# Kernel tuning notes

Hardware: AMD Instinct MI355X
Metric: run time of the kernel (lower is better)

Reference implementation:

```python
import jax, jax.numpy as jnp
import numpy as np

H = 16  # num_attention_heads


def setup_inputs() -> dict:
    key = jax.random.key(0)
    k1, k2, k3 = jax.random.split(key, 3)
    B, S, E = 2, 2048, 1024
    return {
        "hidden_states": jax.random.normal(k1, (B, S, E), dtype=jnp.float32),
        "W_attn": jax.random.normal(k2, (E, 3 * E), dtype=jnp.float32) * 0.02,
        "b_attn": jnp.zeros((3 * E,), dtype=jnp.float32),
        "W_proj": jax.random.normal(k3, (E, E), dtype=jnp.float32) * 0.02,
        "b_proj": jnp.zeros((E,), dtype=jnp.float32),
    }


def reference(hidden_states, W_attn, b_attn, W_proj, b_proj):
    B, S, E = hidden_states.shape
    hd = E // H
    # Conv1D: x @ W + b -> [B, S, 3E]
    qkv = hidden_states @ W_attn + b_attn
    # Faithful to module: _split_heads with 3*head_dim FIRST, then split q/k/v.
    # i.e. per-head slice of size 3*hd is [q_h | k_h | v_h] (interleaved layout).
    qkv = qkv.reshape(B, S, H, 3 * hd).transpose(0, 2, 1, 3)  # [B, H, S, 3*hd]
    q, k, v = jnp.split(qkv, 3, axis=-1)                      # each [B, H, S, hd]
    # scores, scaled by sqrt(head_dim) (value.size(-1) ** 0.5)
    scores = jnp.einsum("bhqd,bhkd->bhqk", q, k) / jnp.asarray(hd, q.dtype) ** 0.5
    # causal mask via where with masked_bias = -10000.0 (not -inf), as in module
    causal = jnp.tril(jnp.ones((S, S), dtype=bool))
    scores = jnp.where(causal, scores, jnp.asarray(-10000.0, scores.dtype))
    attn_weights = jax.nn.softmax(scores, axis=-1)  # dropout p=0 -> identity
    attn_out = jnp.einsum("bhqk,bhkd->bhqd", attn_weights, v)
    attn_out = attn_out.transpose(0, 2, 1, 3).reshape(B, S, E)  # merge heads
    return attn_out @ W_proj + b_proj
```

## Files before the change

### kernel.cpp

```cpp
#include <hip/hip_runtime.h>
#include <hip/hip_bf16.h>


typedef __attribute__((ext_vector_type(4))) float f32x4;
typedef __attribute__((ext_vector_type(8))) short short8;
typedef __attribute__((ext_vector_type(2))) unsigned int uint2v;

#define AS1 __attribute__((address_space(1)))
#define AS3 __attribute__((address_space(3)))

__device__ __forceinline__ void load_lds16(const void* g, void* l) {
    __builtin_amdgcn_global_load_lds((const AS1 void*)g, (AS3 void*)l, 16, 0, 0);
}

__device__ __forceinline__ unsigned short f2bf(float f) {
    union { float f; unsigned int u; } v; v.f = f;
    unsigned int r = v.u + 0x7FFFu + ((v.u >> 16) & 1u);
    return (unsigned short)(r >> 16);
}

__device__ __forceinline__ int cvt_pk_bf16(float lo, float hi) {
    int r;
    asm("v_cvt_pk_bf16_f32 %0, %1, %2" : "=v"(r) : "v"(lo), "v"(hi));
    return r;
}

__device__ __forceinline__ void transpose_tile(
    const float* __restrict__ W, unsigned short* __restrict__ Wt,
    int K, int N, int bx, int by, int t) {
    __shared__ float tile[32][33];
    int k0 = by * 32, n0 = bx * 32;
    int r = t >> 3, c = (t & 7) * 4;
    float4 v = *(const float4*)&W[(size_t)(k0 + r) * N + n0 + c];
    tile[r][c] = v.x; tile[r][c + 1] = v.y; tile[r][c + 2] = v.z; tile[r][c + 3] = v.w;
    __syncthreads();
    int n = t >> 3; int kk = (t & 7) * 4;
    ushort4 o;
    o.x = f2bf(tile[kk + 0][n]);
    o.y = f2bf(tile[kk + 1][n]);
    o.z = f2bf(tile[kk + 2][n]);
    o.w = f2bf(tile[kk + 3][n]);
    *(ushort4*)&Wt[(size_t)(n0 + n) * K + k0 + kk] = o;
}

__global__ __launch_bounds__(256) void prep(
    const float* __restrict__ hs, unsigned short* __restrict__ Xb,
    const float* __restrict__ W_attn, unsigned short* __restrict__ WaT,
    const float* __restrict__ W_proj, unsigned short* __restrict__ WpT) {
    int bid = blockIdx.x, t = threadIdx.x;
    if (bid < 4096) {
        int i = (bid * 256 + t) * 4;
        float4 v = *(const float4*)(hs + i);
        ushort4 o;
        o.x = f2bf(v.x); o.y = f2bf(v.y); o.z = f2bf(v.z); o.w = f2bf(v.w);
        *(ushort4*)(Xb + i) = o;
    } else if (bid < 7168) {
        int r = bid - 4096;
        transpose_tile(W_attn, WaT, 1024, 3072, r % 96, r / 96, t);
    } else {
        int r = bid - 7168;
        transpose_tile(W_proj, WpT, 1024, 1024, r % 32, r / 32, t);
    }
}

__global__ __launch_bounds__(256) void gemm_qkv(
    const unsigned short* __restrict__ A,
    const unsigned short* __restrict__ Bt,
    const float* __restrict__ bias,
    unsigned short* __restrict__ qk, unsigned short* __restrict__ Vt,
    int M, int N, int K) {
    __shared__ unsigned short Sh[8704];
    unsigned short* As = Sh;
    unsigned short* Bs = Sh + 4096;
    unsigned short* Tb = Sh;
    const int t = threadIdx.x, wave = t >> 6, lane = t & 63;
    const int l15 = lane & 15, quad = lane >> 4;
    const int m0 = blockIdx.y * 128, n0 = blockIdx.x * 128;
    const int srow = wave * 32 + (lane >> 2);
    const int sch = (lane & 3) * 8;
    const unsigned short* Ag = A + (size_t)(m0 + srow) * K + sch;
    const unsigned short* Bg = Bt + (size_t)(n0 + srow) * K + sch;
    unsigned short* AsW = &As[wave * 32 * 32];
    unsigned short* BsW = &Bs[wave * 32 * 32];
    const int wm = (wave >> 1) * 64, wn = (wave & 1) * 64;
    f32x4 acc[4][4] = {};
    for (int k0 = 0; k0 < K; k0 += 32) {
        load_lds16(Ag + k0, AsW);
        load_lds16(Ag + k0 + (size_t)16 * K, AsW + 16 * 32);
        load_lds16(Bg + k0, BsW);
        load_lds16(Bg + k0 + (size_t)16 * K, BsW + 16 * 32);
        __syncthreads();
        short8 af[4], bf[4];
#pragma unroll
        for (int i = 0; i < 4; ++i) {
            af[i] = *(const short8*)&As[(wm + i * 16 + l15) * 32 + quad * 8];
            bf[i] = *(const short8*)&Bs[(wn + i * 16 + l15) * 32 + quad * 8];
        }
#pragma unroll
        for (int mt = 0; mt < 4; ++mt)
#pragma unroll
            for (int nt = 0; nt < 4; ++nt)
                acc[mt][nt] = __builtin_amdgcn_mfma_f32_16x16x32_bf16(af[mt], bf[nt], acc[mt][nt], 0, 0, 0);
        __syncthreads();
    }
    const int rem = n0 % 192;
#pragma unroll
    for (int mt = 0; mt < 4; ++mt) {
        int mrow = m0 + wm + mt * 16 + quad * 4;
#pragma unroll
        for (int nt = 0; nt < 4; ++nt) {
            int col = n0 + wn + nt * 16 + l15;
            float bv = bias[col];
            int h = col / 192;
            int j = col - h * 192;
            if (j < 128) {
                float sc = (j < 64) ? 0.125f : 1.0f;
#pragma unroll
                for (int r = 0; r < 4; ++r)
                    qk[(size_t)(mrow + r) * 2048 + h * 128 + j] = f2bf((acc[mt][nt][r] + bv) * sc);
            } else {
                int d = j - 128;
                int s_local = wm + mt * 16 + quad * 4;
                ushort4 pk;
                pk.x = f2bf(acc[mt][nt][0] + bv);
                pk.y = f2bf(acc[mt][nt][1] + bv);
                pk.z = f2bf(acc[mt][nt][2] + bv);
                pk.w = f2bf(acc[mt][nt][3] + bv);
                *(ushort4*)&Tb[d * 136 + s_local] = pk;
            }
        }
    }
    if (rem != 0) {
        __syncthreads();
        int vhalf = (rem == 64) ? 1 : 0;
        int h = (n0 + vhalf * 64) / 192;
        int b = m0 >> 11;
        unsigned short* vbase = Vt + ((size_t)(b * 16 + h) * 64) * 2048 + (m0 & 2047);
        int drow = t >> 4, ch = (t & 15) * 8;
#pragma unroll
        for (int rr = 0; rr < 4; ++rr) {
            int d = rr * 16 + drow;
            *(uint4*)(vbase + (size_t)d * 2048 + ch) = *(const uint4*)&Tb[d * 136 + ch];
        }
    }
}

__global__ __launch_bounds__(256) void gemm_proj(
    const unsigned short* __restrict__ A,
    const unsigned short* __restrict__ Bt,
    const float* __restrict__ bias,
    float* __restrict__ C, int M, int N, int K) {
    __shared__ unsigned short As[128 * 32];
    __shared__ unsigned short Bs[64 * 32];
    const int t = threadIdx.x, wave = t >> 6, lane = t & 63;
    const int l15 = lane & 15, quad = lane >> 4;
    const int m0 = blockIdx.y * 128, n0 = blockIdx.x * 64;
    const int srowA = wave * 32 + (lane >> 2);
    const int sch = (lane & 3) * 8;
    const unsigned short* Ag = A + (size_t)(m0 + srowA) * K + sch;
    const unsigned short* Bg = Bt + (size_t)(n0 + wave * 16 + (lane >> 2)) * K + sch;
    unsigned short* AsW = &As[wave * 32 * 32];
    unsigned short* BsW = &Bs[wave * 16 * 32];
    const int wm = (wave >> 1) * 64, wn = (wave & 1) * 32;
    f32x4 acc[4][2] = {};
    for (int k0 = 0; k0 < K; k0 += 32) {
        load_lds16(Ag + k0, AsW);
        load_lds16(Ag + k0 + (size_t)16 * K, AsW + 16 * 32);
        load_lds16(Bg + k0, BsW);
        __syncthreads();
        short8 af[4], bf[2];
#pragma unroll
        for (int i = 0; i < 4; ++i)
            af[i] = *(const short8*)&As[(wm + i * 16 + l15) * 32 + quad * 8];
#pragma unroll
        for (int i = 0; i < 2; ++i)
            bf[i] = *(const short8*)&Bs[(wn + i * 16 + l15) * 32 + quad * 8];
#pragma unroll
        for (int mt = 0; mt < 4; ++mt)
#pragma unroll
            for (int nt = 0; nt < 2; ++nt)
                acc[mt][nt] = __builtin_amdgcn_mfma_f32_16x16x32_bf16(af[mt], bf[nt], acc[mt][nt], 0, 0, 0);
        __syncthreads();
    }
#pragma unroll
    for (int mt = 0; mt < 4; ++mt) {
        int mrow = m0 + wm + mt * 16 + quad * 4;
#pragma unroll
        for (int nt = 0; nt < 2; ++nt) {
            int col = n0 + wn + nt * 16 + l15;
            float bv = bias[col];
#pragma unroll
            for (int r = 0; r < 4; ++r)
                C[(size_t)(mrow + r) * N + col] = acc[mt][nt][r] + bv;
        }
    }
}

__device__ __forceinline__ void build_af(const int (&pk)[4][2], int qpar, short8 (&af)[2]) {
#pragma unroll
    for (int km = 0; km < 2; ++km) {
        uint2v r0 = __builtin_amdgcn_permlane32_swap(
            (unsigned)pk[2 * km][0], (unsigned)pk[2 * km + 1][0], false, false);
        uint2v r1 = __builtin_amdgcn_permlane32_swap(
            (unsigned)pk[2 * km][1], (unsigned)pk[2 * km + 1][1], false, false);
        int Ap0 = (int)r0[0], Bp0 = (int)r0[1];
        int Ap1 = (int)r1[0], Bp1 = (int)r1[1];
        int z0 = qpar ? Ap0 : Bp0;
        int z1 = qpar ? Ap1 : Bp1;
        int w0 = __builtin_amdgcn_ds_swizzle(z0, 0x401F);
        int w1 = __builtin_amdgcn_ds_swizzle(z1, 0x401F);
        int f0 = qpar ? w0 : Ap0, f1 = qpar ? w1 : Ap1;
        int g0 = qpar ? Bp0 : w0, g1 = qpar ? Bp1 : w1;
        int4 v = {f0, f1, g0, g1};
        af[km] = __builtin_bit_cast(short8, v);
    }
}

__global__ __launch_bounds__(512, 4) void attn3(
    const unsigned short* __restrict__ qk,
    const unsigned short* __restrict__ Vt,
    unsigned short* __restrict__ out) {
    const int S = 2048;
    __shared__ unsigned short Ks[2][64][72];
    __shared__ unsigned short Vts[2][64][72];
    const int t = threadIdx.x, wave = t >> 6, lane = t & 63;
    const int l15 = lane & 15, quad = lane >> 4, qpar = quad & 1;
    const int bid = blockIdx.x;
    const int qt = (bid < 256) ? (15 - (bid >> 5)) : ((bid - 256) >> 5);
    const int bh = bid & 31;
    const int b = bh >> 4, h = bh & 15;
    const unsigned short* qkb = qk + (size_t)b * S * 2048 + h * 128;
    const unsigned short* vtb = Vt + (size_t)bh * 64 * 2048;

    const int q0 = qt * 128 + wave * 16;
    short8 qf[2];
#pragma unroll
    for (int km = 0; km < 2; ++km)
        qf[km] = *(const short8*)(qkb + (size_t)(q0 + l15) * 2048 + km * 32 + quad * 8);
    f32x4 o[4] = {};
    float lrun = 0.f;

    const int srow8 = t >> 3, chunk8 = (t & 7) * 8;
    const int KT = qt * 2 + 2;

    uint4 kreg = *(const uint4*)(qkb + (size_t)srow8 * 2048 + 64 + chunk8);
    uint4 vreg = *(const uint4*)(vtb + (size_t)srow8 * 2048 + chunk8);

    const int qg = q0 + l15;
    const int qmax = q0 + 15;

    for (int kt = 0; kt < KT; ++kt) {
        const int cur = kt & 1;
        *(uint4*)&Ks[cur][srow8][chunk8] = kreg;
        *(uint4*)&Vts[cur][srow8][chunk8] = vreg;
        __syncthreads();
        if (kt + 1 < KT) {
            int kn = (kt + 1) * 64;
            kreg = *(const uint4*)(qkb + (size_t)(kn + srow8) * 2048 + 64 + chunk8);
            vreg = *(const uint4*)(vtb + (size_t)srow8 * 2048 + kn + chunk8);
        }
        const int kb = kt * 64;
        if (kb > qmax) continue;

        f32x4 s[4] = {};
        __builtin_amdgcn_s_setprio(1);
#pragma unroll
        for (int km = 0; km < 2; ++km)
#pragma unroll
            for (int nt = 0; nt < 4; ++nt) {
                short8 kf = *(const short8*)&Ks[cur][nt * 16 + l15][km * 32 + quad * 8];
                s[nt] = __builtin_amdgcn_mfma_f32_16x16x32_bf16(kf, qf[km], s[nt], 0, 0, 0);
            }
        __builtin_amdgcn_s_setprio(0);

        if (kb + 63 > q0) {
            const int ka = kb + quad * 4;
#pragma unroll
            for (int nt = 0; nt < 4; ++nt)
#pragma unroll
                for (int r = 0; r < 4; ++r)
                    if (ka + nt * 16 + r > qg) s[nt][r] = -1e30f;
        }

        int pk[4][2];
        float a0 = 0.f;
#pragma unroll
        for (int nt = 0; nt < 4; ++nt) {
            float pa[4];
#pragma unroll
            for (int r = 0; r < 4; ++r) {
                pa[r] = __expf(s[nt][r]);
                a0 += pa[r];
            }
            pk[nt][0] = cvt_pk_bf16(pa[0], pa[1]);
            pk[nt][1] = cvt_pk_bf16(pa[2], pa[3]);
        }
        lrun += a0;

        short8 af[2];
        build_af(pk, qpar, af);

        __builtin_amdgcn_s_setprio(1);
#pragma unroll
        for (int km = 0; km < 2; ++km)
#pragma unroll
            for (int nt = 0; nt < 4; ++nt) {
                short8 vf = *(const short8*)&Vts[cur][nt * 16 + l15][km * 32 + quad * 8];
                o[nt] = __builtin_amdgcn_mfma_f32_16x16x32_bf16(af[km], vf, o[nt], 0, 0, 0);
            }
        __builtin_amdgcn_s_setprio(0);
    }

    float t0 = lrun + __shfl_xor(lrun, 16);
    t0 += __shfl_xor(t0, 32);
    unsigned short* ob = out + (size_t)b * S * 1024 + h * 64;
#pragma unroll
    for (int r = 0; r < 4; ++r) {
        float i0 = 1.0f / __shfl(t0, quad * 4 + r);
        size_t r0 = (size_t)(q0 + quad * 4 + r) * 1024;
#pragma unroll
        for (int nt = 0; nt < 4; ++nt)
            ob[r0 + nt * 16 + l15] = f2bf(o[nt][r] * i0);
    }
}

extern "C" void kernel_launch(void* const* d_in, const int* in_sizes, int n_in,
                              void* d_out, int out_size, void* d_ws, size_t ws_size,
                              hipStream_t stream) {
    const float* hs     = (const float*)d_in[0];
    const float* W_attn = (const float*)d_in[1];
    const float* b_attn = (const float*)d_in[2];
    const float* W_proj = (const float*)d_in[3];
    const float* b_proj = (const float*)d_in[4];
    float* out = (float*)d_out;

    const int B = 2, S = 2048, E = 1024;
    const int M = B * S;
    const int N3 = 3 * E;

    unsigned short* Xb  = (unsigned short*)d_ws;
    unsigned short* WaT = Xb + (size_t)M * E;
    unsigned short* WpT = WaT + (size_t)N3 * E;
    unsigned short* qkb = WpT + (size_t)E * E;
    unsigned short* Vt  = qkb + (size_t)M * 2048;
    unsigned short* ao  = Vt + (size_t)M * E;

    prep<<<dim3(8192), 256, 0, stream>>>(hs, Xb, W_attn, WaT, W_proj, WpT);

    gemm_qkv<<<dim3(N3 / 128, M / 128), 256, 0, stream>>>(Xb, WaT, b_attn, qkb, Vt, M, N3, E);

    attn3<<<dim3(512), 512, 0, stream>>>(qkb, Vt, ao);

    gemm_proj<<<dim3(E / 64, M / 128), 256, 0, stream>>>(ao, WpT, b_proj, out, M, E, E);
}
```

Before: 184.0 us.

## Double-buffer LDS tiles in QKV and projection GEMMs with MFMA priority boost

Both GEMM kernels now keep two LDS buffers. The next K-slice is fetched with async global-to-LDS loads while MFMAs run on the current slice, so each K step needs one barrier instead of two. The MFMA block is wrapped in s_setprio to favour matrix issue over other waves. The cost is roughly twice the LDS per block, which can lower occupancy. An extra barrier after the QKV loop protects reuse of the LDS transpose buffer.

```diff
diff --git a/kernel.cpp b/kernel.cpp
--- a/kernel.cpp
+++ b/kernel.cpp
@@ -69,10 +69,8 @@
     const float* __restrict__ bias,
     unsigned short* __restrict__ qk, unsigned short* __restrict__ Vt,
     int M, int N, int K) {
-    __shared__ unsigned short Sh[8704];
-    unsigned short* As = Sh;
-    unsigned short* Bs = Sh + 4096;
-    unsigned short* Tb = Sh;
+    __shared__ unsigned short Sh[2][8192];
+    unsigned short* Tb = &Sh[0][0];
     const int t = threadIdx.x, wave = t >> 6, lane = t & 63;
     const int l15 = lane & 15, quad = lane >> 4;
     const int m0 = blockIdx.y * 128, n0 = blockIdx.x * 128;
@@ -80,29 +78,43 @@
     const int sch = (lane & 3) * 8;
     const unsigned short* Ag = A + (size_t)(m0 + srow) * K + sch;
     const unsigned short* Bg = Bt + (size_t)(n0 + srow) * K + sch;
-    unsigned short* AsW = &As[wave * 32 * 32];
-    unsigned short* BsW = &Bs[wave * 32 * 32];
+    const int wOff = wave * 1024;
     const int wm = (wave >> 1) * 64, wn = (wave & 1) * 64;
     f32x4 acc[4][4] = {};
-    for (int k0 = 0; k0 < K; k0 += 32) {
-        load_lds16(Ag + k0, AsW);
-        load_lds16(Ag + k0 + (size_t)16 * K, AsW + 16 * 32);
-        load_lds16(Bg + k0, BsW);
-        load_lds16(Bg + k0 + (size_t)16 * K, BsW + 16 * 32);
+    const int NSTEP = K / 32;
+    load_lds16(Ag, &Sh[0][wOff]);
+    load_lds16(Ag + (size_t)16 * K, &Sh[0][wOff + 512]);
+    load_lds16(Bg, &Sh[0][4096 + wOff]);
+    load_lds16(Bg + (size_t)16 * K, &Sh[0][4096 + wOff + 512]);
+    for (int kt = 0; kt < NSTEP; ++kt) {
+        const int cur = kt & 1;
+        const unsigned short* As = &Sh[cur][0];
+        const unsigned short* Bs = &Sh[cur][4096];
         __syncthreads();
+        if (kt + 1 < NSTEP) {
+            const int k1 = (kt + 1) * 32;
+            unsigned short* An = &Sh[cur ^ 1][0];
+            unsigned short* Bn = &Sh[cur ^ 1][4096];
+            load_lds16(Ag + k1, An + wOff);
+            load_lds16(Ag + k1 + (size_t)16 * K, An + wOff + 512);
+            load_lds16(Bg + k1, Bn + wOff);
+            load_lds16(Bg + k1 + (size_t)16 * K, Bn + wOff + 512);
+        }
         short8 af[4], bf[4];
 #pragma unroll
         for (int i = 0; i < 4; ++i) {
             af[i] = *(const short8*)&As[(wm + i * 16 + l15) * 32 + quad * 8];
             bf[i] = *(const short8*)&Bs[(wn + i * 16 + l15) * 32 + quad * 8];
         }
+        __builtin_amdgcn_s_setprio(1);
 #pragma unroll
         for (int mt = 0; mt < 4; ++mt)
 #pragma unroll
             for (int nt = 0; nt < 4; ++nt)
                 acc[mt][nt] = __builtin_amdgcn_mfma_f32_16x16x32_bf16(af[mt], bf[nt], acc[mt][nt], 0, 0, 0);
-        __syncthreads();
-    }
+        __builtin_amdgcn_s_setprio(0);
+    }
+    __syncthreads();
     const int rem = n0 % 192;
 #pragma unroll
     for (int mt = 0; mt < 4; ++mt) {
@@ -150,8 +162,7 @@
     const unsigned short* __restrict__ Bt,
     const float* __restrict__ bias,
     float* __restrict__ C, int M, int N, int K) {
-    __shared__ unsigned short As[128 * 32];
-    __shared__ unsigned short Bs[64 * 32];
+    __shared__ unsigned short Sh[2][6144];
     const int t = threadIdx.x, wave = t >> 6, lane = t & 63;
     const int l15 = lane & 15, quad = lane >> 4;
     const int m0 = blockIdx.y * 128, n0 = blockIdx.x * 64;
@@ -159,15 +170,24 @@
     const int sch = (lane & 3) * 8;
     const unsigned short* Ag = A + (size_t)(m0 + srowA) * K + sch;
     const unsigned short* Bg = Bt + (size_t)(n0 + wave * 16 + (lane >> 2)) * K + sch;
-    unsigned short* AsW = &As[wave * 32 * 32];
-    unsigned short* BsW = &Bs[wave * 16 * 32];
+    const int aOff = wave * 1024, bOff = wave * 512;
     const int wm = (wave >> 1) * 64, wn = (wave & 1) * 32;
     f32x4 acc[4][2] = {};
-    for (int k0 = 0; k0 < K; k0 += 32) {
-        load_lds16(Ag + k0, AsW);
-        load_lds16(Ag + k0 + (size_t)16 * K, AsW + 16 * 32);
-        load_lds16(Bg + k0, BsW);
+    const int NSTEP = K / 32;
+    load_lds16(Ag, &Sh[0][aOff]);
+    load_lds16(Ag + (size_t)16 * K, &Sh[0][aOff + 512]);
+    load_lds16(Bg, &Sh[0][4096 + bOff]);
+    for (int kt = 0; kt < NSTEP; ++kt) {
+        const int cur = kt & 1;
+        const unsigned short* As = &Sh[cur][0];
+        const unsigned short* Bs = &Sh[cur][4096];
         __syncthreads();
+        if (kt + 1 < NSTEP) {
+            const int k1 = (kt + 1) * 32;
+            load_lds16(Ag + k1, &Sh[cur ^ 1][aOff]);
+            load_lds16(Ag + k1 + (size_t)16 * K, &Sh[cur ^ 1][aOff + 512]);
+            load_lds16(Bg + k1, &Sh[cur ^ 1][4096 + bOff]);
+        }
         short8 af[4], bf[2];
 #pragma unroll
         for (int i = 0; i < 4; ++i)
@@ -175,12 +195,13 @@
 #pragma unroll
         for (int i = 0; i < 2; ++i)
             bf[i] = *(const short8*)&Bs[(wn + i * 16 + l15) * 32 + quad * 8];
+        __builtin_amdgcn_s_setprio(1);
 #pragma unroll
         for (int mt = 0; mt < 4; ++mt)
 #pragma unroll
             for (int nt = 0; nt < 2; ++nt)
                 acc[mt][nt] = __builtin_amdgcn_mfma_f32_16x16x32_bf16(af[mt], bf[nt], acc[mt][nt], 0, 0, 0);
-        __syncthreads();
+        __builtin_amdgcn_s_setprio(0);
     }
 #pragma unroll
     for (int mt = 0; mt < 4; ++mt) {
```

Measured after the change: 176.1 us. 1.04x faster.
